# Kernel tuning notes

Hardware: AMD Instinct MI355X
Metric: run time of the kernel (lower is better)

## Reference

```python
import jax, jax.numpy as jnp
import numpy as np

BATCH = 32768
NUM_CLASSES = 1024  # balanced binary hierarchy => 10 levels, 1023 internal nodes


def setup_inputs() -> dict:
    key = jax.random.key(0)
    outputs = jax.random.normal(key, (BATCH, NUM_CLASSES), dtype=jnp.float32)
    return {"outputs": outputs}


def reference(outputs) -> jnp.ndarray:
    """SoftEmbeddedDecisionRules.forward for a balanced binary hierarchy.

    For every internal node: child logit = mean of raw logits over the child's
    leaf (class) set, softmax over the node's children, then multiply each
    class's running probability by the prob of the branch containing it.
    With a balanced binary tree over C classes, level l has 2^l nodes, each
    child covering a contiguous block of C / 2^(l+1) classes, so the per-node
    Python loop of the original collapses into one reshape+mean+softmax per
    level (log2(C) fused passes total).
    """
    B, C = outputs.shape
    depth = C.bit_length() - 1  # log2(C), static
    class_probs = jnp.ones((B, C), dtype=outputs.dtype)
    for level in range(depth):
        n_nodes = 1 << level
        seg = C // (2 * n_nodes)  # classes per child subtree
        # node logits: mean of raw logits over each child's class block
        node_logits = outputs.reshape(B, n_nodes, 2, seg).mean(axis=-1)  # [B, n, 2]
        probs = jax.nn.softmax(node_logits, axis=-1)  # softmax over children
        # scatter-multiply child prob onto every class in that child's subtree
        expanded = jnp.broadcast_to(probs[..., None], (B, n_nodes, 2, seg)).reshape(B, C)
        class_probs = class_probs * expanded
    return class_probs
```

## Files before the change

kernel.cpp:

```cpp
#include <hip/hip_runtime.h>


#define C 1024

__device__ __forceinline__ float sigd(float d) {
    return 1.0f / (1.0f + __expf(d));
}

__global__ __launch_bounds__(256) void hier_softmax_kernel(
    const float* __restrict__ in, float* __restrict__ out) {
    __shared__ float qsum[4];
    const int row = blockIdx.x;
    const int tid = threadIdx.x;
    const int wave = tid >> 6;

    const float4 v = ((const float4*)(in + (size_t)row * C))[tid];

    const float pA = sigd(v.y - v.x);
    const float pB = sigd(v.w - v.z);
    const float s2a = v.x + v.y, s2b = v.z + v.w;
    const float p8 = sigd((s2b - s2a) * 0.5f);

    float S = s2a + s2b;
    float common = 1.0f;
    float inv = 0.25f;
#pragma unroll
    for (int m = 1; m <= 32; m <<= 1) {
        const float sib = __shfl_xor(S, m, 64);
        common *= sigd((sib - S) * inv);
        S += sib;
        inv *= 0.5f;
    }
    if ((tid & 63) == 0) qsum[wave] = S;
    __syncthreads();
    const float q0 = qsum[0], q1 = qsum[1], q2 = qsum[2], q3 = qsum[3];
    const float topL = sigd(((q2 + q3) - (q0 + q1)) * (1.0f / 512.0f));
    const float pq01 = sigd((q1 - q0) * (1.0f / 256.0f));
    const float pq23 = sigd((q3 - q2) * (1.0f / 256.0f));

    const float pl0 = (wave < 2) ? topL : (1.0f - topL);
    const float pqh = (wave < 2) ? pq01 : pq23;
    const float pl1 = (wave & 1) ? (1.0f - pqh) : pqh;
    common *= pl0 * pl1;

    const float cl = common * p8;
    const float cr = common * (1.0f - p8);
    float4 o;
    o.x = cl * pA;
    o.y = cl * (1.0f - pA);
    o.z = cr * pB;
    o.w = cr * (1.0f - pB);
    ((float4*)(out + (size_t)row * C))[tid] = o;
}

extern "C" void kernel_launch(void* const* d_in, const int* in_sizes, int n_in,
                              void* d_out, int out_size, void* d_ws, size_t ws_size,
                              hipStream_t stream) {
    const float* in = (const float*)d_in[0];
    float* out = (float*)d_out;
    const int B = in_sizes[0] / C;
    hier_softmax_kernel<<<B, 256, 0, stream>>>(in, out);
}
```

Measured before the change: 220.4 us.

## Map one wavefront per row with grid-stride loop and nontemporal stores

Each row is now handled by a single 64-lane wavefront that loads four float4 chunks per lane. The top two tree levels are resolved inside registers, which removes the shared-memory exchange and the block barrier. A persistent grid of 2048 blocks walks the rows with a grid-stride loop, and outputs are written with nontemporal stores to avoid polluting the cache. The cost is more registers per thread and four interleaved shuffle chains per lane.

```diff
diff --git a/kernel.cpp b/kernel.cpp
--- a/kernel.cpp
+++ b/kernel.cpp
@@ -2,55 +2,69 @@
 
 
 #define C 1024
+
+typedef float f4 __attribute__((ext_vector_type(4)));
 
 __device__ __forceinline__ float sigd(float d) {
     return 1.0f / (1.0f + __expf(d));
 }
 
 __global__ __launch_bounds__(256) void hier_softmax_kernel(
-    const float* __restrict__ in, float* __restrict__ out) {
-    __shared__ float qsum[4];
-    const int row = blockIdx.x;
-    const int tid = threadIdx.x;
-    const int wave = tid >> 6;
+    const float* __restrict__ in, float* __restrict__ out, int B) {
+    const int lane = threadIdx.x & 63;
+    const int waveId = (blockIdx.x * blockDim.x + threadIdx.x) >> 6;
+    const int nWaves = (gridDim.x * blockDim.x) >> 6;
 
-    const float4 v = ((const float4*)(in + (size_t)row * C))[tid];
+    for (int row = waveId; row < B; row += nWaves) {
+        const f4* __restrict__ rowp = (const f4*)(in + (size_t)row * C);
 
-    const float pA = sigd(v.y - v.x);
-    const float pB = sigd(v.w - v.z);
-    const float s2a = v.x + v.y, s2b = v.z + v.w;
-    const float p8 = sigd((s2b - s2a) * 0.5f);
+        f4 v[4];
+#pragma unroll
+        for (int q = 0; q < 4; ++q) v[q] = rowp[q * 64 + lane];
 
-    float S = s2a + s2b;
-    float common = 1.0f;
-    float inv = 0.25f;
+        float pA[4], pB[4], p8[4], S[4], common[4];
 #pragma unroll
-    for (int m = 1; m <= 32; m <<= 1) {
-        const float sib = __shfl_xor(S, m, 64);
-        common *= sigd((sib - S) * inv);
-        S += sib;
-        inv *= 0.5f;
+        for (int q = 0; q < 4; ++q) {
+            pA[q] = sigd(v[q].y - v[q].x);
+            pB[q] = sigd(v[q].w - v[q].z);
+            const float s2a = v[q].x + v[q].y;
+            const float s2b = v[q].z + v[q].w;
+            p8[q] = sigd((s2b - s2a) * 0.5f);
+            S[q] = s2a + s2b;
+            common[q] = 1.0f;
+        }
+
+        float inv = 0.25f;
+#pragma unroll
+        for (int m = 1; m <= 32; m <<= 1) {
+#pragma unroll
+            for (int q = 0; q < 4; ++q) {
+                const float sib = __shfl_xor(S[q], m, 64);
+                common[q] *= sigd((sib - S[q]) * inv);
+                S[q] += sib;
+            }
+            inv *= 0.5f;
+        }
+        const float topL = sigd(((S[2] + S[3]) - (S[0] + S[1])) * (1.0f / 512.0f));
+        const float pq01 = sigd((S[1] - S[0]) * (1.0f / 256.0f));
+        const float pq23 = sigd((S[3] - S[2]) * (1.0f / 256.0f));
+        const float lvl01[4] = {topL * pq01, topL * (1.0f - pq01),
+                                (1.0f - topL) * pq23, (1.0f - topL) * (1.0f - pq23)};
+
+        f4* __restrict__ orow = (f4*)(out + (size_t)row * C);
+#pragma unroll
+        for (int q = 0; q < 4; ++q) {
+            const float cm = common[q] * lvl01[q];
+            const float cl = cm * p8[q];
+            const float cr = cm * (1.0f - p8[q]);
+            f4 o;
+            o.x = cl * pA[q];
+            o.y = cl * (1.0f - pA[q]);
+            o.z = cr * pB[q];
+            o.w = cr * (1.0f - pB[q]);
+            __builtin_nontemporal_store(o, orow + q * 64 + lane);
+        }
     }
-    if ((tid & 63) == 0) qsum[wave] = S;
-    __syncthreads();
-    const float q0 = qsum[0], q1 = qsum[1], q2 = qsum[2], q3 = qsum[3];
-    const float topL = sigd(((q2 + q3) - (q0 + q1)) * (1.0f / 512.0f));
-    const float pq01 = sigd((q1 - q0) * (1.0f / 256.0f));
-    const float pq23 = sigd((q3 - q2) * (1.0f / 256.0f));
-
-    const float pl0 = (wave < 2) ? topL : (1.0f - topL);
-    const float pqh = (wave < 2) ? pq01 : pq23;
-    const float pl1 = (wave & 1) ? (1.0f - pqh) : pqh;
-    common *= pl0 * pl1;
-
-    const float cl = common * p8;
-    const float cr = common * (1.0f - p8);
-    float4 o;
-    o.x = cl * pA;
-    o.y = cl * (1.0f - pA);
-    o.z = cr * pB;
-    o.w = cr * (1.0f - pB);
-    ((float4*)(out + (size_t)row * C))[tid] = o;
 }
 
 extern "C" void kernel_launch(void* const* d_in, const int* in_sizes, int n_in,
@@ -59,5 +73,5 @@
     const float* in = (const float*)d_in[0];
     float* out = (float*)d_out;
     const int B = in_sizes[0] / C;
-    hier_softmax_kernel<<<B, 256, 0, stream>>>(in, out);
+    hier_softmax_kernel<<<2048, 256, 0, stream>>>(in, out, B);
 }
```

Measured after the change: 231.5 us. +5.0%, slower.
